# Optimization experiments

Hardware: AMD Instinct MI355X
Metric: run time of the kernel (lower is better)

Reference implementation:

```python
import jax, jax.numpy as jnp
import numpy as np

B, L, D, H = 2, 1024, 1024, 16
HD = D // H  # head_dim = 64


def setup_inputs() -> dict:
    key = jax.random.key(0)
    ks = jax.random.split(key, 6)
    s = 1.0 / np.sqrt(D)
    return {
        "x": jax.random.normal(ks[0], (B, L, D), jnp.float32),
        "structure_bias": jax.random.normal(ks[1], (B, L, D), jnp.float32),
        # weights stored as [in, out] (transposed vs torch nn.Linear)
        "Wqkv": jax.random.normal(ks[2], (D, 3 * D), jnp.float32) * s,
        "bqkv": jnp.zeros((3 * D,), jnp.float32),
        "Ws": jax.random.normal(ks[3], (D, D), jnp.float32) * s,
        "bs": jnp.zeros((D,), jnp.float32),
        "Wo": jax.random.normal(ks[4], (D, D), jnp.float32) * s,
        "bo": jnp.zeros((D,), jnp.float32),
    }


def reference(x, structure_bias, Wqkv, bqkv, Ws, bs, Wo, bo):
    b, l, d = x.shape
    # qkv: [B, L, 3, H, HD] -> (3, B, H, L, HD)
    qkv = (x @ Wqkv + bqkv).reshape(b, l, 3, H, HD).transpose(2, 0, 3, 1, 4)
    q, k, v = qkv[0], qkv[1], qkv[2]
    scale = 1.0 / jnp.sqrt(jnp.float32(HD))
    attn = jnp.einsum("bhld,bhmd->bhlm", q, k) * scale  # [B,H,L,L]
    # structure bias: Linear then view(B, 1, L, L); requires L == feature_dim
    sw = (structure_bias @ Ws + bs).reshape(b, 1, l, l)
    attn = jax.nn.softmax(attn + sw, axis=-1)
    out = jnp.einsum("bhlm,bhmd->bhld", attn, v)  # [B,H,L,HD]
    out = out.transpose(0, 2, 1, 3).reshape(b, l, d)
    return out @ Wo + bo
```

## Files before the change

kernel.cpp:

```cpp
#include <hip/hip_runtime.h>
#include <stdint.h>
#include <stddef.h>


typedef float f32x4 __attribute__((ext_vector_type(4)));
typedef short s16x8 __attribute__((ext_vector_type(8)));
typedef unsigned short u16x8 __attribute__((ext_vector_type(8)));
typedef unsigned short u16x4 __attribute__((ext_vector_type(4)));

__device__ inline unsigned short f2bf(float f) {
    unsigned u = __builtin_bit_cast(unsigned, f);
    u += 0x7fffu + ((u >> 16) & 1u);
    return (unsigned short)(u >> 16);
}

__device__ inline f32x4 mfma16(s16x8 a, s16x8 b, f32x4 c) {
    return __builtin_amdgcn_mfma_f32_16x16x32_bf16(a, b, c, 0, 0, 0);
}

__device__ inline void gld_lds16(const void* g, const void* lds_base) {
    __builtin_amdgcn_global_load_lds(
        (const __attribute__((address_space(1))) void*)(uintptr_t)g,
        (__attribute__((address_space(3))) void*)(unsigned)(uintptr_t)lds_base,
        16, 0, 0);
}

__global__ __launch_bounds__(256) void prep_k(const float* __restrict__ x,
                                              const float* __restrict__ sb,
                                              const float* __restrict__ Wqkv,
                                              const float* __restrict__ Ws,
                                              const float* __restrict__ Wo,
                                              unsigned short* __restrict__ xb,
                                              unsigned short* __restrict__ sbb,
                                              unsigned short* __restrict__ wqkvt,
                                              unsigned short* __restrict__ wst,
                                              unsigned short* __restrict__ wot) {
    __shared__ float tile[64][65];
    const int blk = blockIdx.x, t = threadIdx.x;
    if (blk < 2048) {
        const float* src = (blk < 1024) ? x : sb;
        unsigned short* dst = (blk < 1024) ? xb : sbb;
        int i = (blk & 1023) * 256 + t;
        const float4* s4 = (const float4*)src;
        float4 a = s4[2 * i], b = s4[2 * i + 1];
        u16x8 o;
        o[0] = f2bf(a.x); o[1] = f2bf(a.y); o[2] = f2bf(a.z); o[3] = f2bf(a.w);
        o[4] = f2bf(b.x); o[5] = f2bf(b.y); o[6] = f2bf(b.z); o[7] = f2bf(b.w);
        *(u16x8*)(dst + (size_t)i * 8) = o;
        return;
    }
    int tt = blk - 2048;
    const float* W; unsigned short* Wt; int N, n0, k0;
    if (tt < 768)       { W = Wqkv; Wt = wqkvt; N = 3072; n0 = (tt % 48) * 64; k0 = (tt / 48) * 64; }
    else if (tt < 1024) { tt -= 768;  W = Ws; Wt = wst; N = 1024; n0 = (tt & 15) * 64; k0 = (tt >> 4) * 64; }
    else                { tt -= 1024; W = Wo; Wt = wot; N = 1024; n0 = (tt & 15) * 64; k0 = (tt >> 4) * 64; }
    const int lr = t >> 4, lc = (t & 15) * 4;
#pragma unroll
    for (int rr = 0; rr < 4; rr++) {
        int r = lr + rr * 16;
        float4 v = *(const float4*)(W + (size_t)(k0 + r) * N + n0 + lc);
        tile[r][lc] = v.x; tile[r][lc + 1] = v.y; tile[r][lc + 2] = v.z; tile[r][lc + 3] = v.w;
    }
    __syncthreads();
    const int wn = t >> 3, wk = (t & 7) * 8;
#pragma unroll
    for (int rr = 0; rr < 2; rr++) {
        int n = wn + rr * 32;
        u16x8 o;
#pragma unroll
        for (int j = 0; j < 8; j++) o[j] = f2bf(tile[wk + j][n]);
        *(u16x8*)(Wt + (size_t)(n0 + n) * 1024 + k0 + wk) = o;
    }
}

template <int EPI>
__global__ __launch_bounds__(256, 3) void gemm_k(const unsigned short* __restrict__ A,
                                                 const unsigned short* __restrict__ Bt,
                                                 const float* __restrict__ bias,
                                                 unsigned short* __restrict__ q,
                                                 unsigned short* __restrict__ kk_,
                                                 unsigned short* __restrict__ vt,
                                                 float* __restrict__ outf) {
    __shared__ unsigned short lA[2][4096];
    __shared__ unsigned short lB[2][8192];
    const int t = threadIdx.x;
    const int wave = t >> 6, lane = t & 63, c = lane & 15, g = lane >> 4;
    const int bn0 = blockIdx.x * 128, bm0 = blockIdx.y * 64;
    const int wc = wave * 32;

    size_t aoff[2], boff[4];
#pragma unroll
    for (int j = 0; j < 2; j++) {
        int s = j * 256 + t, row = s >> 3, ch = (s & 7) ^ (row & 7);
        aoff[j] = (size_t)(bm0 + row) * 1024 + ch * 8;
    }
#pragma unroll
    for (int j = 0; j < 4; j++) {
        int s = j * 256 + t, row = s >> 3, ch = (s & 7) ^ (row & 7);
        boff[j] = (size_t)(bn0 + row) * 1024 + ch * 8;
    }
    char* lAb0 = (char*)lA[0]; char* lBb0 = (char*)lB[0];

#define GSTAGE(buf, kt)                                                                  \
    do {                                                                                 \
        _Pragma("unroll")                                                                \
        for (int j = 0; j < 2; j++)                                                      \
            gld_lds16(A + aoff[j] + (kt), lAb0 + (buf) * 8192 + j * 4096 + wave * 1024); \
        _Pragma("unroll")                                                                \
        for (int j = 0; j < 4; j++)                                                      \
            gld_lds16(Bt + boff[j] + (kt), lBb0 + (buf) * 16384 + j * 4096 + wave * 1024);\
    } while (0)

    f32x4 acc[4][2];
#pragma unroll
    for (int i = 0; i < 4; i++)
#pragma unroll
        for (int j = 0; j < 2; j++) acc[i][j] = {0.f, 0.f, 0.f, 0.f};

    GSTAGE(0, 0);
    for (int ks = 0; ks < 16; ++ks) {
        __syncthreads();
        if (ks < 15) GSTAGE((ks + 1) & 1, (ks + 1) * 64);
        const char* aB = lAb0 + (ks & 1) * 8192;
        const char* bB = lBb0 + (ks & 1) * 16384;
#pragma unroll
        for (int kk2 = 0; kk2 < 2; ++kk2) {
            s16x8 af[4], bfr[2];
#pragma unroll
            for (int i = 0; i < 4; i++) {
                int r_ = i * 16 + c;
                af[i] = *(const s16x8*)(aB + r_ * 128 + (((kk2 * 4 + g) ^ (r_ & 7)) << 4));
            }
#pragma unroll
            for (int j = 0; j < 2; j++) {
                int r_ = wc + j * 16 + c;
                bfr[j] = *(const s16x8*)(bB + r_ * 128 + (((kk2 * 4 + g) ^ (r_ & 7)) << 4));
            }
#pragma unroll
            for (int i = 0; i < 4; i++)
#pragma unroll
                for (int j = 0; j < 2; j++)
                    acc[i][j] = mfma16(af[i], bfr[j], acc[i][j]);
        }
    }
#undef GSTAGE

#pragma unroll
    for (int i = 0; i < 4; i++) {
#pragma unroll
        for (int j = 0; j < 2; j++) {
            const int n = bn0 + wc + j * 16 + c;
            const float bv = bias[n];
#pragma unroll
            for (int r = 0; r < 4; r++) {
                const int m = bm0 + i * 16 + g * 4 + r;
                float v = acc[i][j][r] + bv;
                if (EPI == 0) {
                    const int sel = n >> 10, h = (n >> 6) & 15, d = n & 63;
                    const int b_ = m >> 10, l_ = m & 1023;
                    const size_t bh = (size_t)((b_ << 4) + h);
                    unsigned short hv = f2bf(v);
                    if (sel == 0)      q[(bh * 1024 + l_) * 64 + d] = hv;
                    else if (sel == 1) kk_[(bh * 1024 + l_) * 64 + d] = hv;
                    else               vt[(bh * 64 + d) * 1024 + l_] = hv;
                } else {
                    outf[(size_t)m * 1024 + n] = v;
                }
            }
        }
    }
}

__global__ __launch_bounds__(256, 2) void attn_k(const unsigned short* __restrict__ q,
                                                 const unsigned short* __restrict__ k,
                                                 const unsigned short* __restrict__ vt,
                                                 const float* __restrict__ sw,
                                                 unsigned short* __restrict__ ctx) {
    __shared__ unsigned short kbuf[2][4096];
    __shared__ unsigned short vbuf[2][4096];
    __shared__ unsigned short lP[4][640];
    const int t = threadIdx.x, wave = t >> 6, lane = t & 63, c = lane & 15, g = lane >> 4;
    const int blk = blockIdx.x;
    const int qt = blk & 15, bh = blk >> 4, b_ = bh >> 4, h = bh & 15;
    const int qr = qt * 64 + wave * 16;

    const unsigned short* qbase = q + ((size_t)bh * 1024 + qr) * 64;
    s16x8 qf0 = *(const s16x8*)(qbase + (size_t)c * 64 + g * 8);
    s16x8 qf1 = *(const s16x8*)(qbase + (size_t)c * 64 + 32 + g * 8);

    const unsigned short* kg = k + (size_t)bh * 65536;
    const unsigned short* vg = vt + (size_t)bh * 65536;
    const float* swrow = sw + ((size_t)b_ * 1024 + qr + c) * 1024;

    const int s0 = wave * 128 + lane, s1 = s0 + 64;
    const int r0 = s0 >> 3, ch0 = (s0 & 7) ^ (r0 & 7);
    const int r1 = s1 >> 3, ch1 = (s1 & 7) ^ (r1 & 7);

    const float SC  = 0.125f * 1.4426950408889634f;
    const float L2E = 1.4426950408889634f;

    float mr = -1e30f, lr = 0.0f;
    f32x4 acc[4];
#pragma unroll
    for (int nf = 0; nf < 4; nf++) acc[nf] = {0.f, 0.f, 0.f, 0.f};
    unsigned short* wp = lP[wave];
    const int swz = (c & 7);

#define STAGE(buf, kv0)                                                                     \
    do {                                                                                    \
        gld_lds16(kg + (size_t)((kv0) + r0) * 64 + ch0 * 8, (char*)kbuf[buf] + wave * 2048);            \
        gld_lds16(kg + (size_t)((kv0) + r1) * 64 + ch1 * 8, (char*)kbuf[buf] + wave * 2048 + 1024);     \
        gld_lds16(vg + (size_t)r0 * 1024 + (kv0) + ch0 * 8, (char*)vbuf[buf] + wave * 2048);            \
        gld_lds16(vg + (size_t)r1 * 1024 + (kv0) + ch1 * 8, (char*)vbuf[buf] + wave * 2048 + 1024);     \
    } while (0)

    STAGE(0, 0);
    __syncthreads();

    int cur = 0;
    for (int it = 0; it < 16; ++it) {
        const int kv0 = it * 64;
        if (it < 15) STAGE(cur ^ 1, kv0 + 64);
        float4 sws[4];
#pragma unroll
        for (int j = 0; j < 4; j++) sws[j] = *(const float4*)(swrow + kv0 + j * 16 + 4 * g);

        const char* kB = (const char*)kbuf[cur];
        const char* vB = (const char*)vbuf[cur];
#pragma unroll
        for (int ks2 = 0; ks2 < 2; ++ks2) {
            s16x8 kc0 = *(const s16x8*)(kB + ((ks2 * 32 + c) << 7) + (((0 + g) ^ swz) << 4));
            s16x8 kc1 = *(const s16x8*)(kB + ((ks2 * 32 + c) << 7) + (((4 + g) ^ swz) << 4));
            s16x8 kc2 = *(const s16x8*)(kB + ((ks2 * 32 + 16 + c) << 7) + (((0 + g) ^ swz) << 4));
            s16x8 kc3 = *(const s16x8*)(kB + ((ks2 * 32 + 16 + c) << 7) + (((4 + g) ^ swz) << 4));

            __builtin_amdgcn_s_setprio(1);
            f32x4 ss0 = {0.f, 0.f, 0.f, 0.f}, ss1 = {0.f, 0.f, 0.f, 0.f};
            ss0 = mfma16(kc0, qf0, ss0); ss0 = mfma16(kc1, qf1, ss0);
            ss1 = mfma16(kc2, qf0, ss1); ss1 = mfma16(kc3, qf1, ss1);
            __builtin_amdgcn_s_setprio(0);

            float4 swa = sws[2 * ks2], swb = sws[2 * ks2 + 1];
            float z0[4], z1[4];
#pragma unroll
            for (int r = 0; r < 4; r++) {
                z0[r] = ss0[r] * SC + (&swa.x)[r] * L2E;
                z1[r] = ss1[r] * SC + (&swb.x)[r] * L2E;
            }
            float tm = fmaxf(fmaxf(fmaxf(z0[0], z0[1]), fmaxf(z0[2], z0[3])),
                             fmaxf(fmaxf(z1[0], z1[1]), fmaxf(z1[2], z1[3])));
            tm = fmaxf(tm, __shfl_xor(tm, 16, 64));
            tm = fmaxf(tm, __shfl_xor(tm, 32, 64));

            const bool need = __any((int)(tm > mr + 8.0f));
            float mn = mr, f = 1.0f;
            if (need) { mn = fmaxf(mr, tm); f = __builtin_amdgcn_exp2f(mr - mn); }

            float p0[4], p1[4];
#pragma unroll
            for (int r = 0; r < 4; r++) {
                p0[r] = __builtin_amdgcn_exp2f(z0[r] - mn);
                p1[r] = __builtin_amdgcn_exp2f(z1[r] - mn);
            }
            float rs = (p0[0] + p0[1]) + (p0[2] + p0[3]) + (p1[0] + p1[1]) + (p1[2] + p1[3]);
            rs += __shfl_xor(rs, 16, 64);
            rs += __shfl_xor(rs, 32, 64);

            if (need) {
                mr = mn;
                lr = lr * f + rs;
#pragma unroll
                for (int nf = 0; nf < 4; nf++)
#pragma unroll
                    for (int r = 0; r < 4; r++) acc[nf][r] *= f;
            } else {
                lr += rs;
            }

            u16x4 w0, w1;
#pragma unroll
            for (int r = 0; r < 4; r++) { w0[r] = f2bf(p0[r]); w1[r] = f2bf(p1[r]); }
            *(u16x4*)(wp + c * 40 + 4 * g) = w0;
            *(u16x4*)(wp + c * 40 + 16 + 4 * g) = w1;
            s16x8 ap = *(const s16x8*)((const char*)wp + c * 80 + g * 16);

            __builtin_amdgcn_s_setprio(1);
#pragma unroll
            for (int nf = 0; nf < 4; nf++) {
                s16x8 vf = *(const s16x8*)(vB + ((nf * 16 + c) << 7) + ((((ks2 << 2) + g) ^ swz) << 4));
                acc[nf] = mfma16(vf, ap, acc[nf]);
            }
            __builtin_amdgcn_s_setprio(0);
        }
        __syncthreads();
        cur ^= 1;
    }
#undef STAGE

    float inv = 1.0f / lr;
#pragma unroll
    for (int nf = 0; nf < 4; nf++)
#pragma unroll
        for (int r = 0; r < 4; r++) acc[nf][r] *= inv;

    __syncthreads();
    float* scr = (wave < 2) ? ((float*)kbuf + wave * 1088)
                            : ((float*)vbuf + (wave - 2) * 1088);
#pragma unroll
    for (int nf = 0; nf < 4; nf++)
#pragma unroll
        for (int r = 0; r < 4; r++)
            scr[(nf * 16 + 4 * g + r) * 17 + c] = acc[nf][r];
    __syncthreads();
    u16x8 o0, o1;
#pragma unroll
    for (int j = 0; j < 8; j++) o0[j] = f2bf(scr[(g * 16 + j) * 17 + c]);
#pragma unroll
    for (int j = 0; j < 8; j++) o1[j] = f2bf(scr[(g * 16 + 8 + j) * 17 + c]);
    unsigned short* dst = ctx + ((size_t)(b_ << 10) + qr + c) * 1024 + (h << 6) + g * 16;
    *(u16x8*)dst = o0;
    *(u16x8*)(dst + 8) = o1;
}

extern "C" void kernel_launch(void* const* d_in, const int* in_sizes, int n_in,
                              void* d_out, int out_size, void* d_ws, size_t ws_size,
                              hipStream_t stream) {
    const float* x    = (const float*)d_in[0];
    const float* sb   = (const float*)d_in[1];
    const float* Wqkv = (const float*)d_in[2];
    const float* bqkv = (const float*)d_in[3];
    const float* Ws   = (const float*)d_in[4];
    const float* bs   = (const float*)d_in[5];
    const float* Wo   = (const float*)d_in[6];
    const float* bo   = (const float*)d_in[7];
    float* out = (float*)d_out;

    char* ws = (char*)d_ws;
    unsigned short* xb    = (unsigned short*)(ws);
    unsigned short* sbb   = (unsigned short*)(ws + ((size_t)4 << 20));
    unsigned short* wqkvt = (unsigned short*)(ws + ((size_t)8 << 20));
    unsigned short* wst   = (unsigned short*)(ws + ((size_t)14 << 20));
    unsigned short* wot   = (unsigned short*)(ws + ((size_t)16 << 20));
    unsigned short* qb    = (unsigned short*)(ws + ((size_t)18 << 20));
    unsigned short* kb    = (unsigned short*)(ws + ((size_t)22 << 20));
    unsigned short* vtb   = (unsigned short*)(ws + ((size_t)26 << 20));
    float*          swf   = (float*)        (ws + ((size_t)30 << 20));
    unsigned short* ctxb  = (unsigned short*)(ws + ((size_t)38 << 20));

    prep_k<<<dim3(3328), dim3(256), 0, stream>>>(x, sb, Wqkv, Ws, Wo,
                                                 xb, sbb, wqkvt, wst, wot);
    gemm_k<0><<<dim3(24, 32), dim3(256), 0, stream>>>(xb, wqkvt, bqkv, qb, kb, vtb, (float*)nullptr);
    gemm_k<1><<<dim3(8, 32), dim3(256), 0, stream>>>(sbb, wst, bs,
                                                     (unsigned short*)nullptr, (unsigned short*)nullptr,
                                                     (unsigned short*)nullptr, swf);
    attn_k<<<dim3(512), dim3(256), 0, stream>>>(qb, kb, vtb, swf, ctxb);
    gemm_k<1><<<dim3(8, 32), dim3(256), 0, stream>>>(ctxb, wot, bo,
                                                     (unsigned short*)nullptr, (unsigned short*)nullptr,
                                                     (unsigned short*)nullptr, out);
}
```

Baseline: 92.37 us.

## Merge QKV and structure-bias GEMMs into one launch; row-sum softmax via MFMA

The QKV projection and the structure-bias projection now run in a single kernel launch with larger 128x128 tiles and a 2x2 wave layout. The output GEMM becomes its own specialized kernel. MFMA blocks in both GEMMs are wrapped in s_setprio. In attention, the per-row softmax denominator is computed by an extra MFMA against a ones vector, replacing the shuffle reductions. This removes one launch and the cross-lane reduction work, but adds an MFMA per step, and the denominator is now summed from bf16-rounded probabilities. The larger tiles also change occupancy.

```diff
diff --git a/kernel.cpp b/kernel.cpp
--- a/kernel.cpp
+++ b/kernel.cpp
@@ -73,14 +73,116 @@
     }
 }
 
-template <int EPI>
-__global__ __launch_bounds__(256, 3) void gemm_k(const unsigned short* __restrict__ A,
-                                                 const unsigned short* __restrict__ Bt,
-                                                 const float* __restrict__ bias,
-                                                 unsigned short* __restrict__ q,
-                                                 unsigned short* __restrict__ kk_,
-                                                 unsigned short* __restrict__ vt,
-                                                 float* __restrict__ outf) {
+__global__ __launch_bounds__(256, 2) void gemm01_k(const unsigned short* __restrict__ xb,
+                                                   const unsigned short* __restrict__ wqkvt,
+                                                   const float* __restrict__ bqkv,
+                                                   const unsigned short* __restrict__ sbb,
+                                                   const unsigned short* __restrict__ wst,
+                                                   const float* __restrict__ bs,
+                                                   unsigned short* __restrict__ q,
+                                                   unsigned short* __restrict__ kk_,
+                                                   unsigned short* __restrict__ vt,
+                                                   float* __restrict__ swf) {
+    __shared__ unsigned short lA[2][8192];
+    __shared__ unsigned short lB[2][8192];
+    const int blk = blockIdx.x, t = threadIdx.x;
+    const int wave = t >> 6, lane = t & 63, c = lane & 15, g = lane >> 4;
+    const int wr = (wave >> 1) * 64, wc = (wave & 1) * 64;
+
+    const unsigned short* A;
+    const unsigned short* Bt;
+    const float* bias;
+    int bn0, bm0, epi;
+    if (blk < 384) { A = xb;  Bt = wqkvt; bias = bqkv; epi = 0;
+                     bn0 = (blk % 24) * 128; bm0 = (blk / 24) * 128; }
+    else           { int bb = blk - 384; A = sbb; Bt = wst; bias = bs; epi = 1;
+                     bn0 = (bb & 7) * 128; bm0 = (bb >> 3) * 128; }
+
+    size_t aoff[4], boff[4];
+#pragma unroll
+    for (int j = 0; j < 4; j++) {
+        int s = j * 256 + t, row = s >> 3, ch = (s & 7) ^ (row & 7);
+        aoff[j] = (size_t)(bm0 + row) * 1024 + ch * 8;
+        boff[j] = (size_t)(bn0 + row) * 1024 + ch * 8;
+    }
+    char* lAb0 = (char*)lA[0]; char* lBb0 = (char*)lB[0];
+
+#define GS128(buf, kt)                                                                    \
+    do {                                                                                  \
+        _Pragma("unroll")                                                                 \
+        for (int j = 0; j < 4; j++)                                                       \
+            gld_lds16(A + aoff[j] + (kt), lAb0 + (buf) * 16384 + j * 4096 + wave * 1024); \
+        _Pragma("unroll")                                                                 \
+        for (int j = 0; j < 4; j++)                                                       \
+            gld_lds16(Bt + boff[j] + (kt), lBb0 + (buf) * 16384 + j * 4096 + wave * 1024);\
+    } while (0)
+
+    f32x4 acc[4][4];
+#pragma unroll
+    for (int i = 0; i < 4; i++)
+#pragma unroll
+        for (int j = 0; j < 4; j++) acc[i][j] = {0.f, 0.f, 0.f, 0.f};
+
+    GS128(0, 0);
+    for (int ks = 0; ks < 16; ++ks) {
+        __syncthreads();
+        if (ks < 15) GS128((ks + 1) & 1, (ks + 1) * 64);
+        const char* aB = lAb0 + (ks & 1) * 16384;
+        const char* bB = lBb0 + (ks & 1) * 16384;
+#pragma unroll
+        for (int kk2 = 0; kk2 < 2; ++kk2) {
+            s16x8 af[4], bfr[4];
+#pragma unroll
+            for (int i = 0; i < 4; i++) {
+                int r_ = wr + i * 16 + c;
+                af[i] = *(const s16x8*)(aB + r_ * 128 + (((kk2 * 4 + g) ^ (r_ & 7)) << 4));
+            }
+#pragma unroll
+            for (int j = 0; j < 4; j++) {
+                int r_ = wc + j * 16 + c;
+                bfr[j] = *(const s16x8*)(bB + r_ * 128 + (((kk2 * 4 + g) ^ (r_ & 7)) << 4));
+            }
+            __builtin_amdgcn_s_setprio(1);
+#pragma unroll
+            for (int i = 0; i < 4; i++)
+#pragma unroll
+                for (int j = 0; j < 4; j++)
+                    acc[i][j] = mfma16(af[i], bfr[j], acc[i][j]);
+            __builtin_amdgcn_s_setprio(0);
+        }
+    }
+#undef GS128
+
+#pragma unroll
+    for (int i = 0; i < 4; i++) {
+#pragma unroll
+        for (int j = 0; j < 4; j++) {
+            const int n = bn0 + wc + j * 16 + c;
+            const float bv = bias[n];
+#pragma unroll
+            for (int r = 0; r < 4; r++) {
+                const int m = bm0 + wr + i * 16 + g * 4 + r;
+                float v = acc[i][j][r] + bv;
+                if (epi == 0) {
+                    const int sel = n >> 10, h = (n >> 6) & 15, d = n & 63;
+                    const int b_ = m >> 10, l_ = m & 1023;
+                    const size_t bh = (size_t)((b_ << 4) + h);
+                    unsigned short hv = f2bf(v);
+                    if (sel == 0)      q[(bh * 1024 + l_) * 64 + d] = hv;
+                    else if (sel == 1) kk_[(bh * 1024 + l_) * 64 + d] = hv;
+                    else               vt[(bh * 64 + d) * 1024 + l_] = hv;
+                } else {
+                    swf[(size_t)m * 1024 + n] = v;
+                }
+            }
+        }
+    }
+}
+
+__global__ __launch_bounds__(256, 3) void gemmo_k(const unsigned short* __restrict__ A,
+                                                  const unsigned short* __restrict__ Bt,
+                                                  const float* __restrict__ bias,
+                                                  float* __restrict__ outf) {
     __shared__ unsigned short lA[2][4096];
     __shared__ unsigned short lB[2][8192];
     const int t = threadIdx.x;
@@ -136,11 +238,13 @@
                 int r_ = wc + j * 16 + c;
                 bfr[j] = *(const s16x8*)(bB + r_ * 128 + (((kk2 * 4 + g) ^ (r_ & 7)) << 4));
             }
+            __builtin_amdgcn_s_setprio(1);
 #pragma unroll
             for (int i = 0; i < 4; i++)
 #pragma unroll
                 for (int j = 0; j < 2; j++)
                     acc[i][j] = mfma16(af[i], bfr[j], acc[i][j]);
+            __builtin_amdgcn_s_setprio(0);
         }
     }
 #undef GSTAGE
@@ -154,18 +258,7 @@
 #pragma unroll
             for (int r = 0; r < 4; r++) {
                 const int m = bm0 + i * 16 + g * 4 + r;
-                float v = acc[i][j][r] + bv;
-                if (EPI == 0) {
-                    const int sel = n >> 10, h = (n >> 6) & 15, d = n & 63;
-                    const int b_ = m >> 10, l_ = m & 1023;
-                    const size_t bh = (size_t)((b_ << 4) + h);
-                    unsigned short hv = f2bf(v);
-                    if (sel == 0)      q[(bh * 1024 + l_) * 64 + d] = hv;
-                    else if (sel == 1) kk_[(bh * 1024 + l_) * 64 + d] = hv;
-                    else               vt[(bh * 64 + d) * 1024 + l_] = hv;
-                } else {
-                    outf[(size_t)m * 1024 + n] = v;
-                }
+                outf[(size_t)m * 1024 + n] = acc[i][j][r] + bv;
             }
         }
     }
@@ -199,8 +292,12 @@
     const float SC  = 0.125f * 1.4426950408889634f;
     const float L2E = 1.4426950408889634f;
 
-    float mr = -1e30f, lr = 0.0f;
+    const short one_bf = (short)0x3F80;
+    const s16x8 ones = { one_bf, one_bf, one_bf, one_bf, one_bf, one_bf, one_bf, one_bf };
+
+    float mr = -1e30f;
     f32x4 acc[4];
+    f32x4 accl = {0.f, 0.f, 0.f, 0.f};
 #pragma unroll
     for (int nf = 0; nf < 4; nf++) acc[nf] = {0.f, 0.f, 0.f, 0.f};
     unsigned short* wp = lP[wave];
@@ -253,28 +350,23 @@
             tm = fmaxf(tm, __shfl_xor(tm, 32, 64));
 
             const bool need = __any((int)(tm > mr + 8.0f));
-            float mn = mr, f = 1.0f;
-            if (need) { mn = fmaxf(mr, tm); f = __builtin_amdgcn_exp2f(mr - mn); }
+            float mn = mr;
+            if (need) {
+                mn = fmaxf(mr, tm);
+                float f = __builtin_amdgcn_exp2f(mr - mn);
+                mr = mn;
+                accl *= f;
+#pragma unroll
+                for (int nf = 0; nf < 4; nf++)
+#pragma unroll
+                    for (int r = 0; r < 4; r++) acc[nf][r] *= f;
+            }
 
             float p0[4], p1[4];
 #pragma unroll
             for (int r = 0; r < 4; r++) {
                 p0[r] = __builtin_amdgcn_exp2f(z0[r] - mn);
                 p1[r] = __builtin_amdgcn_exp2f(z1[r] - mn);
-            }
-            float rs = (p0[0] + p0[1]) + (p0[2] + p0[3]) + (p1[0] + p1[1]) + (p1[2] + p1[3]);
-            rs += __shfl_xor(rs, 16, 64);
-            rs += __shfl_xor(rs, 32, 64);
-
-            if (need) {
-                mr = mn;
-                lr = lr * f + rs;
-#pragma unroll
-                for (int nf = 0; nf < 4; nf++)
-#pragma unroll
-                    for (int r = 0; r < 4; r++) acc[nf][r] *= f;
-            } else {
-                lr += rs;
             }
 
             u16x4 w0, w1;
@@ -285,6 +377,7 @@
             s16x8 ap = *(const s16x8*)((const char*)wp + c * 80 + g * 16);
 
             __builtin_amdgcn_s_setprio(1);
+            accl = mfma16(ones, ap, accl);
 #pragma unroll
             for (int nf = 0; nf < 4; nf++) {
                 s16x8 vf = *(const s16x8*)(vB + ((nf * 16 + c) << 7) + ((((ks2 << 2) + g) ^ swz) << 4));
@@ -297,7 +390,7 @@
     }
 #undef STAGE
 
-    float inv = 1.0f / lr;
+    float inv = 1.0f / accl[0];
 #pragma unroll
     for (int nf = 0; nf < 4; nf++)
 #pragma unroll
@@ -349,12 +442,8 @@
 
     prep_k<<<dim3(3328), dim3(256), 0, stream>>>(x, sb, Wqkv, Ws, Wo,
                                                  xb, sbb, wqkvt, wst, wot);
-    gemm_k<0><<<dim3(24, 32), dim3(256), 0, stream>>>(xb, wqkvt, bqkv, qb, kb, vtb, (float*)nullptr);
-    gemm_k<1><<<dim3(8, 32), dim3(256), 0, stream>>>(sbb, wst, bs,
-                                                     (unsigned short*)nullptr, (unsigned short*)nullptr,
-                                                     (unsigned short*)nullptr, swf);
+    gemm01_k<<<dim3(512), dim3(256), 0, stream>>>(xb, wqkvt, bqkv, sbb, wst, bs,
+                                                  qb, kb, vtb, swf);
     attn_k<<<dim3(512), dim3(256), 0, stream>>>(qb, kb, vtb, swf, ctxb);
-    gemm_k<1><<<dim3(8, 32), dim3(256), 0, stream>>>(ctxb, wot, bo,
-                                                     (unsigned short*)nullptr, (unsigned short*)nullptr,
-                                                     (unsigned short*)nullptr, out);
-}
+    gemmo_k<<<dim3(8, 32), dim3(256), 0, stream>>>(ctxb, wot, bo, out);
+}
```

After: 85.93 us. -7.0%, faster.
